# Performance work log

Measured on AMD Instinct MI355X. Metric: run time of the kernel, lower is better.

The kernel has to match this reference:

```python
import jax, jax.numpy as jnp
import numpy as np

EXP_SCALING = 10.0
N_HEAD = 16
KEY_SCALE_MAX = float(np.log(2 ** 16 - 1))


def setup_inputs() -> dict:
    key = jax.random.key(0)
    k1, k2, k3, k4 = jax.random.split(key, 4)
    B, T, C = 8, 2048, 1024
    nh = N_HEAD
    x = jax.random.normal(k1, (B, T, C), dtype=jnp.float32)
    Wk_weight = jax.random.normal(k2, (C, C), dtype=jnp.float32) * (1.0 / np.sqrt(C))
    # faithful to torch init: linspace(0.5, 5, nh)/10 and ones/10
    leaky_key_beta = (jnp.linspace(0.5, 5.0, nh, dtype=jnp.float32) / EXP_SCALING).reshape(1, nh, 1, 1)
    key_scale = jnp.ones((1, nh, 1, 1), dtype=jnp.float32) / EXP_SCALING
    return {"x": x, "Wk_weight": Wk_weight, "leaky_key_beta": leaky_key_beta,
            "key_scale": key_scale, "scale_pow": 1}


def reference(x, Wk_weight, leaky_key_beta, key_scale, scale_pow):
    B, T, C = x.shape
    nh = N_HEAD
    hs = C // nh
    # W_k projection + head split (the torch transpose/view dance is the standard split)
    k = (x @ Wk_weight.T).reshape(B, T, nh, hs).transpose(0, 2, 1, 3)  # (B, nh, T, hs)
    # LeakyAvg: coef[t, s] = exp(-(t - s) * beta_h) for s <= t, else 0
    beta = jnp.abs(leaky_key_beta).reshape(nh, 1, 1) * EXP_SCALING  # (nh, 1, 1)
    idx = jnp.arange(T)
    diff = idx[:, None] - idx[None, :]                # (T, T), >=0 below diag
    mask = diff >= 0
    diff_c = jnp.where(mask, diff, 0).astype(x.dtype)
    coef = jnp.exp(-diff_c * beta) * mask.astype(x.dtype)  # (nh, T, T) lower-triangular
    k = jnp.einsum('hts,bhsd->bhtd', coef, k)         # causal decay-weighted sum
    # L2 normalize along head dim
    k = k / (jnp.linalg.norm(k, axis=-1, keepdims=True) + 1e-10)
    # per-head learned scale, clamped in log-space
    scale = jnp.exp(jnp.minimum(scale_pow * EXP_SCALING * key_scale, KEY_SCALE_MAX))
    return k * scale
```

## Files before the change

kernel.cpp:

```cpp
#include <hip/hip_runtime.h>
#include <hip/hip_bf16.h>
#include <stdint.h>

#define B_SZ   8
#define T_SEQ  2048
#define C_DIM  1024
#define NH     16
#define HS     64
#define M_DIM  (B_SZ * T_SEQ)
#define EXP_SC 10.0f
#define KS_MAX 11.090339630053288f

typedef _Float16 f16;
typedef __attribute__((ext_vector_type(8))) _Float16 f16x8;
typedef __attribute__((ext_vector_type(4))) float f32x4;

__global__ void cast_two(const float* __restrict__ xin, f16* __restrict__ xout, int n8x,
                         const float* __restrict__ win, f16* __restrict__ wout, int n8w) {
  int stride = gridDim.x * blockDim.x;
  int t0 = blockIdx.x * blockDim.x + threadIdx.x;
  for (int i = t0; i < n8x; i += stride) {
    const float* p = xin + (size_t)i * 8;
    float4 a = *(const float4*)p;
    float4 b = *(const float4*)(p + 4);
    f16x8 o;
    o[0] = (f16)a.x; o[1] = (f16)a.y; o[2] = (f16)a.z; o[3] = (f16)a.w;
    o[4] = (f16)b.x; o[5] = (f16)b.y; o[6] = (f16)b.z; o[7] = (f16)b.w;
    *(f16x8*)(xout + (size_t)i * 8) = o;
  }
  for (int i = t0; i < n8w; i += stride) {
    const float* p = win + (size_t)i * 8;
    float4 a = *(const float4*)p;
    float4 b = *(const float4*)(p + 4);
    f16x8 o;
    o[0] = (f16)a.x; o[1] = (f16)a.y; o[2] = (f16)a.z; o[3] = (f16)a.w;
    o[4] = (f16)b.x; o[5] = (f16)b.y; o[6] = (f16)b.z; o[7] = (f16)b.w;
    *(f16x8*)(wout + (size_t)i * 8) = o;
  }
}

__device__ __forceinline__ void gl_lds16(const f16* g, const f16* l) {
  __builtin_amdgcn_global_load_lds(
      (const __attribute__((address_space(1))) void*)(uintptr_t)(const void*)g,
      (__attribute__((address_space(3))) void*)(uintptr_t)(const void*)l,
      16, 0, 0);
}

__global__ __launch_bounds__(256, 2)
void gemm_bt_f16(const f16* __restrict__ A,
                 const f16* __restrict__ Bt,
                 float* __restrict__ C) {
  __shared__ f16 As[2][128 * 32];
  __shared__ f16 Bs[2][128 * 32];

  const int tid = threadIdx.x;
  const int w = tid >> 6, l = tid & 63;

  const int q = blockIdx.x;
  const int wgid = (q & 7) * 128 + (q >> 3);
  const int bm = wgid >> 3;
  const int bn = wgid & 7;

  const int wm = w >> 1, wn = w & 1;

  const f32x4 zero = {0.f, 0.f, 0.f, 0.f};
  f32x4 acc[4][4];
#pragma unroll
  for (int i = 0; i < 4; ++i)
#pragma unroll
    for (int j = 0; j < 4; ++j) acc[i][j] = zero;

  const f16* Ag = A + (size_t)(bm * 128) * C_DIM;
  const f16* Bg = Bt + (size_t)(bn * 128) * C_DIM;

  const int r0  = (w * 64 + l) >> 2;
  const int c8  = ((w * 64 + l) & 3) << 3;
  const int lo0 = (w * 64 + l) * 8;

  const int fr = l & 15;
  const int fk = l >> 4;

#define STAGE(buf, k0)                                                   \
  do {                                                                   \
    gl_lds16(Ag + (size_t)r0 * C_DIM + (k0) + c8,        As[buf] + lo0); \
    gl_lds16(Bg + (size_t)r0 * C_DIM + (k0) + c8,        Bs[buf] + lo0); \
    gl_lds16(Ag + (size_t)(r0 + 64) * C_DIM + (k0) + c8, As[buf] + lo0 + 2048); \
    gl_lds16(Bg + (size_t)(r0 + 64) * C_DIM + (k0) + c8, Bs[buf] + lo0 + 2048); \
  } while (0)

  STAGE(0, 0);
  __syncthreads();

  int cur = 0;
  for (int step = 0; step < 32; ++step) {
    if (step + 1 < 32) STAGE(cur ^ 1, (step + 1) * 32);

    f16x8 af[4], bfr[4];
#pragma unroll
    for (int i = 0; i < 4; ++i)
      af[i] = *(const f16x8*)(As[cur] + (wm * 64 + i * 16 + fr) * 32 + fk * 8);
#pragma unroll
    for (int j = 0; j < 4; ++j)
      bfr[j] = *(const f16x8*)(Bs[cur] + (wn * 64 + j * 16 + fr) * 32 + fk * 8);
#pragma unroll
    for (int i = 0; i < 4; ++i)
#pragma unroll
      for (int j = 0; j < 4; ++j)
        acc[i][j] = __builtin_amdgcn_mfma_f32_16x16x32_f16(af[i], bfr[j],
                                                           acc[i][j], 0, 0, 0);

    __syncthreads();
    cur ^= 1;
  }
#undef STAGE

  const int orow0 = bm * 128 + wm * 64 + (l >> 4) * 4;
  const int ocol0 = bn * 128 + wn * 64 + (l & 15);
#pragma unroll
  for (int i = 0; i < 4; ++i)
#pragma unroll
    for (int j = 0; j < 4; ++j)
#pragma unroll
      for (int r = 0; r < 4; ++r)
        C[(size_t)(orow0 + i * 16 + r) * C_DIM + ocol0 + j * 16] = acc[i][j][r];
}

__global__ __launch_bounds__(256)
void scan_norm(const float* __restrict__ kbuf,
               const float* __restrict__ beta_p,
               const float* __restrict__ ks_p,
               const int* __restrict__ sp_p,
               float* __restrict__ out) {
  const int l = threadIdx.x & 63;
  const int gw = blockIdx.x * 4 + (threadIdx.x >> 6);
  const int c = gw & 31;
  const int h = (gw >> 5) & 15;
  const int b = gw >> 9;

  const float beta = fabsf(beta_p[h]) * EXP_SC;
  const float a = expf(-beta);
  const float sp = (float)sp_p[0];
  const float scale = expf(fminf(sp * EXP_SC * ks_p[h], KS_MAX));

  const float* kp = kbuf + (size_t)b * T_SEQ * C_DIM + h * HS + l;
  float* op = out + ((size_t)(b * NH + h) * T_SEQ) * HS + l;

  const int t0 = c * 64;
  float y = 0.f;
  int s = (t0 >= 64) ? (t0 - 64) : 0;
#pragma unroll 8
  for (; s < t0; ++s)
    y = fmaf(a, y, kp[(size_t)s * C_DIM]);

#pragma unroll 4
  for (int t = t0; t < t0 + 64; ++t) {
    y = fmaf(a, y, kp[(size_t)t * C_DIM]);
    float sq = y * y;
#pragma unroll
    for (int m = 1; m < 64; m <<= 1)
      sq += __shfl_xor(sq, m, 64);
    float nrm = sqrtf(sq) + 1e-10f;
    op[(size_t)t * HS] = y * (scale / nrm);
  }
}

extern "C" void kernel_launch(void* const* d_in, const int* in_sizes, int n_in,
                              void* d_out, int out_size, void* d_ws, size_t ws_size,
                              hipStream_t stream) {
  const float* x      = (const float*)d_in[0];
  const float* Wk     = (const float*)d_in[1];
  const float* beta   = (const float*)d_in[2];
  const float* kscale = (const float*)d_in[3];
  const int*   spow   = (const int*)d_in[4];
  float* out = (float*)d_out;

  f16* x_h = (f16*)d_ws;
  f16* W_h = x_h + (size_t)M_DIM * C_DIM;
  float* kbuf = (float*)(W_h + (size_t)C_DIM * C_DIM);

  cast_two<<<2048, 256, 0, stream>>>(x, x_h, (M_DIM * C_DIM) / 8,
                                     Wk, W_h, (C_DIM * C_DIM) / 8);
  gemm_bt_f16<<<dim3((M_DIM / 128) * (C_DIM / 128)), 256, 0, stream>>>(x_h, W_h, kbuf);
  scan_norm<<<1024, 256, 0, stream>>>(kbuf, beta, kscale, spow, out);
}
```

Measured before the change: 205.2 us.

## Rewrite GEMM as 256x256 tile, 8-wave ping-pong schedule with swizzled LDS

The projection GEMM moves from 128x128 tiles with 4 waves and K-step 32 to 256x256 tiles with 8 waves, K-step 64 and an XOR-swizzled LDS layout. Each K iteration is split into four MFMA phases separated by barriers, with s_setprio raising priority around the MFMA bursts and global-to-LDS loads for the next stage issued between them. The goals are more reuse per loaded tile, fewer LDS bank conflicts, and better overlap of memory traffic with matrix math. In exchange it uses much more LDS (128 KB per block) and more accumulator registers, and the whole grid is only 256 blocks.

```diff
diff --git a/kernel.cpp b/kernel.cpp
--- a/kernel.cpp
+++ b/kernel.cpp
@@ -46,78 +46,130 @@
       16, 0, 0);
 }
 
-__global__ __launch_bounds__(256, 2)
-void gemm_bt_f16(const f16* __restrict__ A,
-                 const f16* __restrict__ Bt,
-                 float* __restrict__ C) {
-  __shared__ f16 As[2][128 * 32];
-  __shared__ f16 Bs[2][128 * 32];
+__global__ __launch_bounds__(512, 2)
+void gemm_bt_f16_8p(const f16* __restrict__ A,
+                    const f16* __restrict__ Bt,
+                    float* __restrict__ C) {
+  __shared__ f16 As[2][2][128 * 64];
+  __shared__ f16 Bs[2][2][128 * 64];
 
   const int tid = threadIdx.x;
   const int w = tid >> 6, l = tid & 63;
+  const int wm = w >> 2, wn = w & 3;
 
   const int q = blockIdx.x;
-  const int wgid = (q & 7) * 128 + (q >> 3);
-  const int bm = wgid >> 3;
-  const int bn = wgid & 7;
-
-  const int wm = w >> 1, wn = w & 1;
-
-  const f32x4 zero = {0.f, 0.f, 0.f, 0.f};
-  f32x4 acc[4][4];
-#pragma unroll
-  for (int i = 0; i < 4; ++i)
-#pragma unroll
-    for (int j = 0; j < 4; ++j) acc[i][j] = zero;
-
-  const f16* Ag = A + (size_t)(bm * 128) * C_DIM;
-  const f16* Bg = Bt + (size_t)(bn * 128) * C_DIM;
-
-  const int r0  = (w * 64 + l) >> 2;
-  const int c8  = ((w * 64 + l) & 3) << 3;
-  const int lo0 = (w * 64 + l) * 8;
+  const int wgid = (q & 7) * 32 + (q >> 3);
+  const int bm = wgid >> 2;
+  const int bn = wgid & 3;
+
+  const int srow = l >> 3;
+  const int sswz = (((l & 7) ^ srow)) << 3;
+  const size_t a_lane = (size_t)(bm * 256 + w * 8 + srow) * C_DIM + sswz;
+  const size_t b_lane = (size_t)(bn * 256 + w * 8 + srow) * C_DIM + sswz;
+  const int lds_w = w * 512;
 
   const int fr = l & 15;
   const int fk = l >> 4;
-
-#define STAGE(buf, k0)                                                   \
-  do {                                                                   \
-    gl_lds16(Ag + (size_t)r0 * C_DIM + (k0) + c8,        As[buf] + lo0); \
-    gl_lds16(Bg + (size_t)r0 * C_DIM + (k0) + c8,        Bs[buf] + lo0); \
-    gl_lds16(Ag + (size_t)(r0 + 64) * C_DIM + (k0) + c8, As[buf] + lo0 + 2048); \
-    gl_lds16(Bg + (size_t)(r0 + 64) * C_DIM + (k0) + c8, Bs[buf] + lo0 + 2048); \
+  const int ck0 = ((fk) ^ (l & 7)) << 3;
+  const int ck1 = ((4 + fk) ^ (l & 7)) << 3;
+
+  const f32x4 zero = {0.f, 0.f, 0.f, 0.f};
+  f32x4 acc[8][4];
+#pragma unroll
+  for (int i = 0; i < 8; ++i)
+#pragma unroll
+    for (int j = 0; j < 4; ++j) acc[i][j] = zero;
+
+  f16x8 af[4][2], b0[2][2], b1[2][2];
+
+#define STAGE_A(buf, kt) do {                                                \
+    size_t ko = (size_t)(kt) * 64;                                           \
+    gl_lds16(A + a_lane + ko,                         &As[buf][0][lds_w]);        \
+    gl_lds16(A + a_lane + ko + (size_t) 64 * C_DIM,   &As[buf][0][lds_w + 4096]); \
+    gl_lds16(A + a_lane + ko + (size_t)128 * C_DIM,   &As[buf][1][lds_w]);        \
+    gl_lds16(A + a_lane + ko + (size_t)192 * C_DIM,   &As[buf][1][lds_w + 4096]); \
   } while (0)
-
-  STAGE(0, 0);
+#define STAGE_B(buf, kt) do {                                                \
+    size_t ko = (size_t)(kt) * 64;                                           \
+    gl_lds16(Bt + b_lane + ko,                        &Bs[buf][0][lds_w]);        \
+    gl_lds16(Bt + b_lane + ko + (size_t) 64 * C_DIM,  &Bs[buf][0][lds_w + 4096]); \
+    gl_lds16(Bt + b_lane + ko + (size_t)128 * C_DIM,  &Bs[buf][1][lds_w]);        \
+    gl_lds16(Bt + b_lane + ko + (size_t)192 * C_DIM,  &Bs[buf][1][lds_w + 4096]); \
+  } while (0)
+
+#define MFMA16(mi, ni, BREG) do {                                            \
+    _Pragma("unroll") for (int kk = 0; kk < 2; ++kk)                         \
+    _Pragma("unroll") for (int i = 0; i < 4; ++i)                            \
+    _Pragma("unroll") for (int j = 0; j < 2; ++j)                            \
+      acc[(mi)*4 + i][(ni)*2 + j] = __builtin_amdgcn_mfma_f32_16x16x32_f16(  \
+          af[i][kk], BREG[j][kk], acc[(mi)*4 + i][(ni)*2 + j], 0, 0, 0);     \
+  } while (0)
+
+  STAGE_A(0, 0); STAGE_B(0, 0);
   __syncthreads();
 
-  int cur = 0;
-  for (int step = 0; step < 32; ++step) {
-    if (step + 1 < 32) STAGE(cur ^ 1, (step + 1) * 32);
-
-    f16x8 af[4], bfr[4];
-#pragma unroll
-    for (int i = 0; i < 4; ++i)
-      af[i] = *(const f16x8*)(As[cur] + (wm * 64 + i * 16 + fr) * 32 + fk * 8);
-#pragma unroll
-    for (int j = 0; j < 4; ++j)
-      bfr[j] = *(const f16x8*)(Bs[cur] + (wn * 64 + j * 16 + fr) * 32 + fk * 8);
-#pragma unroll
-    for (int i = 0; i < 4; ++i)
-#pragma unroll
-      for (int j = 0; j < 4; ++j)
-        acc[i][j] = __builtin_amdgcn_mfma_f32_16x16x32_f16(af[i], bfr[j],
-                                                           acc[i][j], 0, 0, 0);
-
-    __syncthreads();
-    cur ^= 1;
-  }
-#undef STAGE
-
-  const int orow0 = bm * 128 + wm * 64 + (l >> 4) * 4;
-  const int ocol0 = bn * 128 + wn * 64 + (l & 15);
-#pragma unroll
-  for (int i = 0; i < 4; ++i)
+  for (int kt = 0; kt < 16; ++kt) {
+    const int cur = kt & 1;
+    const f16* Ab = &As[cur][wm][0];
+    const f16* Bb = &Bs[cur][wn >> 1][(wn & 1) * 4096];
+
+#pragma unroll
+    for (int i = 0; i < 4; ++i) {
+      af[i][0] = *(const f16x8*)(Ab + (i * 16 + fr) * 64 + ck0);
+      af[i][1] = *(const f16x8*)(Ab + (i * 16 + fr) * 64 + ck1);
+    }
+#pragma unroll
+    for (int j = 0; j < 2; ++j) {
+      b0[j][0] = *(const f16x8*)(Bb + (j * 16 + fr) * 64 + ck0);
+      b0[j][1] = *(const f16x8*)(Bb + (j * 16 + fr) * 64 + ck1);
+    }
+    if (kt < 15) STAGE_A(cur ^ 1, kt + 1);
+    __builtin_amdgcn_s_barrier();
+    asm volatile("s_waitcnt lgkmcnt(0)" ::: "memory");
+    __builtin_amdgcn_s_setprio(1);
+    MFMA16(0, 0, b0);
+    __builtin_amdgcn_s_setprio(0);
+    __builtin_amdgcn_s_barrier();
+
+#pragma unroll
+    for (int j = 0; j < 2; ++j) {
+      b1[j][0] = *(const f16x8*)(Bb + ((2 + j) * 16 + fr) * 64 + ck0);
+      b1[j][1] = *(const f16x8*)(Bb + ((2 + j) * 16 + fr) * 64 + ck1);
+    }
+    if (kt < 15) STAGE_B(cur ^ 1, kt + 1);
+    __builtin_amdgcn_s_barrier();
+    asm volatile("s_waitcnt lgkmcnt(0)" ::: "memory");
+    __builtin_amdgcn_s_setprio(1);
+    MFMA16(0, 1, b1);
+    __builtin_amdgcn_s_setprio(0);
+    __builtin_amdgcn_s_barrier();
+
+#pragma unroll
+    for (int i = 0; i < 4; ++i) {
+      af[i][0] = *(const f16x8*)(Ab + (64 + i * 16 + fr) * 64 + ck0);
+      af[i][1] = *(const f16x8*)(Ab + (64 + i * 16 + fr) * 64 + ck1);
+    }
+    __builtin_amdgcn_s_barrier();
+    asm volatile("s_waitcnt lgkmcnt(0)" ::: "memory");
+    __builtin_amdgcn_s_setprio(1);
+    MFMA16(1, 1, b1);
+    __builtin_amdgcn_s_setprio(0);
+    __builtin_amdgcn_s_barrier();
+
+    __builtin_amdgcn_s_setprio(1);
+    MFMA16(1, 0, b0);
+    __builtin_amdgcn_s_setprio(0);
+    asm volatile("s_waitcnt vmcnt(0)" ::: "memory");
+    __builtin_amdgcn_s_barrier();
+  }
+#undef STAGE_A
+#undef STAGE_B
+#undef MFMA16
+
+  const int orow0 = bm * 256 + wm * 128 + (l >> 4) * 4;
+  const int ocol0 = bn * 256 + wn * 64 + (l & 15);
+#pragma unroll
+  for (int i = 0; i < 8; ++i)
 #pragma unroll
     for (int j = 0; j < 4; ++j)
 #pragma unroll
@@ -180,6 +232,6 @@
 
   cast_two<<<2048, 256, 0, stream>>>(x, x_h, (M_DIM * C_DIM) / 8,
                                      Wk, W_h, (C_DIM * C_DIM) / 8);
-  gemm_bt_f16<<<dim3((M_DIM / 128) * (C_DIM / 128)), 256, 0, stream>>>(x_h, W_h, kbuf);
+  gemm_bt_f16_8p<<<dim3((M_DIM / 256) * (C_DIM / 256)), 512, 0, stream>>>(x_h, W_h, kbuf);
   scan_norm<<<1024, 256, 0, stream>>>(kbuf, beta, kscale, spow, out);
 }
```

Result: faster. 198.2 us (-3.4%).
